# Kernel tuning notes

Hardware: AMD Instinct MI355X
Metric: run time of the kernel (lower is better)

## Reference

```python
import jax, jax.numpy as jnp
import numpy as np

B, C, H, W = 8, 256, 200, 200
N = 256
OUT = 7  # out_size


def setup_inputs() -> dict:
    key = jax.random.key(0)
    kf, kb = jax.random.split(key)
    feature_map = jax.random.normal(kf, (B, C, H, W), dtype=jnp.float32)
    # integer box coords; sort (lo,hi) pairs so x1<=x2, y1<=y2 as the torch
    # slicing semantics require for a non-empty ROI
    raw = jax.random.randint(kb, (B, N, 2, 2), 0, W)
    raw = jnp.sort(raw, axis=-1)
    x1 = raw[..., 0, 0]; x2 = raw[..., 0, 1]
    y1 = raw[..., 1, 0]; y2 = raw[..., 1, 1]
    proposals = jnp.stack([x1, y1, x2, y2], axis=-1).astype(jnp.int32)
    return {"feature_map": feature_map, "proposals": proposals}


def reference(feature_map, proposals):
    # Vectorized equivalent of: per-box clamp -> integer slice -> bilinear
    # F.interpolate(size=(OUT,OUT), align_corners=False).
    Bf, Cf, Hf, Wf = feature_map.shape
    S = OUT
    boxes = proposals.reshape(-1, 4)            # [R,4], R = B*N (loop order: batch, then box)
    R = boxes.shape[0]
    bx1 = jnp.clip(boxes[:, 0], 0, Wf - 1)
    by1 = jnp.clip(boxes[:, 1], 0, Hf - 1)
    bx2 = jnp.clip(boxes[:, 2], 0, Wf - 1)
    by2 = jnp.clip(boxes[:, 3], 0, Hf - 1)
    h = by2 - by1 + 1                            # ROI height (int)
    w = bx2 - bx1 + 1
    # PyTorch bilinear (align_corners=False): src = max((dst+0.5)*scale - 0.5, 0)
    grid = jnp.arange(S, dtype=jnp.float32) + 0.5           # [S]
    src_y = jnp.maximum(grid[None, :] * (h.astype(jnp.float32)[:, None] / S) - 0.5, 0.0)  # [R,S]
    src_x = jnp.maximum(grid[None, :] * (w.astype(jnp.float32)[:, None] / S) - 0.5, 0.0)
    y0f = jnp.floor(src_y); x0f = jnp.floor(src_x)
    wy = src_y - y0f; wx = src_x - x0f                       # bilinear lambdas [R,S]
    y0 = y0f.astype(jnp.int32); x0 = x0f.astype(jnp.int32)
    y1i = jnp.minimum(y0 + 1, (h - 1)[:, None])
    x1i = jnp.minimum(x0 + 1, (w - 1)[:, None])
    # absolute feature-map indices
    ya0 = by1[:, None] + y0;  ya1 = by1[:, None] + y1i       # [R,S]
    xa0 = bx1[:, None] + x0;  xa1 = bx1[:, None] + x1i
    bidx = jnp.arange(R, dtype=jnp.int32) // N               # [R] batch of each ROI
    fm = jnp.transpose(feature_map, (0, 2, 3, 1))            # [B,H,W,C] channels-last gather

    def gather(ya, xa):
        return fm[bidx[:, None, None], ya[:, :, None], xa[:, None, :]]  # [R,S,S,C]

    wy_ = wy[:, :, None, None]
    wx_ = wx[:, None, :, None]
    out = ((1 - wy_) * (1 - wx_) * gather(ya0, xa0)
           + (1 - wy_) * wx_ * gather(ya0, xa1)
           + wy_ * (1 - wx_) * gather(ya1, xa0)
           + wy_ * wx_ * gather(ya1, xa1))                    # [R,S,S,C]
    return jnp.transpose(out, (0, 3, 1, 2))                   # [R,C,S,S]
```

## Files before the change

### kernel.cpp

```cpp
#include <hip/hip_runtime.h>


#define C_DIM 256
#define H_DIM 200
#define W_DIM 200
#define S_DIM 7
#define N_ROI 256
#define NXCD  8

__global__ __launch_bounds__(256) void roialign_kernel(
    const float* __restrict__ fm,
    const int*   __restrict__ props,
    float*       __restrict__ out,
    int R)
{
    const int bid = blockIdx.x;
    const int r = (bid & (NXCD - 1)) * (R / NXCD) + (bid >> 3);
    const int b = r >> 8;

    int bx1 = props[r * 4 + 0];
    int by1 = props[r * 4 + 1];
    int bx2 = props[r * 4 + 2];
    int by2 = props[r * 4 + 3];
    bx1 = min(max(bx1, 0), W_DIM - 1);
    by1 = min(max(by1, 0), H_DIM - 1);
    bx2 = min(max(bx2, 0), W_DIM - 1);
    by2 = min(max(by2, 0), H_DIM - 1);
    const int h = by2 - by1 + 1;
    const int w = bx2 - bx1 + 1;

    const int l  = threadIdx.x & 63;
    const int wv = threadIdx.x >> 6;
    const bool active = (l < S_DIM * S_DIM);

    const int sy = l / 7;
    const int sx = l - sy * 7;

    float src_y = fmaxf(((float)sy + 0.5f) * (float)h * (1.0f / S_DIM) - 0.5f, 0.0f);
    float src_x = fmaxf(((float)sx + 0.5f) * (float)w * (1.0f / S_DIM) - 0.5f, 0.0f);
    const float y0f = floorf(src_y);
    const float x0f = floorf(src_x);
    const float wy = src_y - y0f;
    const float wx = src_x - x0f;
    const int y0 = (int)y0f;
    const int x0 = (int)x0f;
    const int y1 = min(y0 + 1, h - 1);
    const int x1 = min(x0 + 1, w - 1);
    const int ya0 = by1 + y0, ya1 = by1 + y1;
    const int xa0 = bx1 + x0, xa1 = bx1 + x1;

    const int o00 = ya0 * W_DIM + xa0;
    const int o01 = ya0 * W_DIM + xa1;
    const int o10 = ya1 * W_DIM + xa0;
    const int o11 = ya1 * W_DIM + xa1;
    const float w00 = (1.0f - wy) * (1.0f - wx);
    const float w01 = (1.0f - wy) * wx;
    const float w10 = wy * (1.0f - wx);
    const float w11 = wy * wx;

    const float* base = fm + ((size_t)b * C_DIM + wv) * (size_t)(H_DIM * W_DIM);
    float*       ob   = out + ((size_t)r * C_DIM + wv) * (S_DIM * S_DIM) + l;

    #pragma unroll 4
    for (int c = wv; c < C_DIM; c += 4) {
        if (active) {
            const float v00 = base[o00];
            const float v01 = base[o01];
            const float v10 = base[o10];
            const float v11 = base[o11];
            *ob = v00 * w00 + v01 * w01 + v10 * w10 + v11 * w11;
        }
        base += 4 * (size_t)(H_DIM * W_DIM);
        ob   += 4 * (S_DIM * S_DIM);
    }
}

extern "C" void kernel_launch(void* const* d_in, const int* in_sizes, int n_in,
                              void* d_out, int out_size, void* d_ws, size_t ws_size,
                              hipStream_t stream)
{
    const float* fm    = (const float*)d_in[0];
    const int*   props = (const int*)d_in[1];
    float*       out   = (float*)d_out;

    const int R = in_sizes[1] / 4;
    roialign_kernel<<<R, 256, 0, stream>>>(fm, props, out, R);
}
```

Measured before the change: 696.9 us.

## Stage half channel planes in LDS and compute all ROI bins per channel

The grid is reorganized so each block owns one (batch, channel, half-plane) tile instead of one ROI. The block streams 100 or 101 rows of the feature plane into LDS with float4 loads, then every thread loops over ROI×bin items and does the bilinear taps from LDS. Bins are split between the two halves by their top sample row. This replaces scattered global gathers, which re-read the same data many times, with one coalesced read of the feature map. In exchange, each block uses about 80 KB of LDS, which limits occupancy, output writes become strided across ROIs, and box and weight math is recomputed in every channel block.

```diff
diff --git a/kernel.cpp b/kernel.cpp
--- a/kernel.cpp
+++ b/kernel.cpp
@@ -1,77 +1,92 @@
 #include <hip/hip_runtime.h>
 
 
+#define B_DIM 8
 #define C_DIM 256
 #define H_DIM 200
 #define W_DIM 200
 #define S_DIM 7
-#define N_ROI 256
-#define NXCD  8
+#define NBINS (S_DIM * S_DIM)
+#define NROI  256
+#define THREADS 512
+#define ROWS_HALF0 101
+#define ROWS_HALF1 100
+#define LDS_BYTES (ROWS_HALF0 * W_DIM * 4)
 
-__global__ __launch_bounds__(256) void roialign_kernel(
+__global__ __launch_bounds__(THREADS) void roialign_kernel(
     const float* __restrict__ fm,
     const int*   __restrict__ props,
-    float*       __restrict__ out,
-    int R)
+    float*       __restrict__ out)
 {
-    const int bid = blockIdx.x;
-    const int r = (bid & (NXCD - 1)) * (R / NXCD) + (bid >> 3);
-    const int b = r >> 8;
+    extern __shared__ float sPlane[];
 
-    int bx1 = props[r * 4 + 0];
-    int by1 = props[r * 4 + 1];
-    int bx2 = props[r * 4 + 2];
-    int by2 = props[r * 4 + 3];
-    bx1 = min(max(bx1, 0), W_DIM - 1);
-    by1 = min(max(by1, 0), H_DIM - 1);
-    bx2 = min(max(bx2, 0), W_DIM - 1);
-    by2 = min(max(by2, 0), H_DIM - 1);
-    const int h = by2 - by1 + 1;
-    const int w = bx2 - bx1 + 1;
+    const int bid  = blockIdx.x;
+    const int half = bid & 1;
+    const int c    = (bid >> 1) & (C_DIM - 1);
+    const int b    = bid >> 9;
 
-    const int l  = threadIdx.x & 63;
-    const int wv = threadIdx.x >> 6;
-    const bool active = (l < S_DIM * S_DIM);
+    const int r0      = half ? 100 : 0;
+    const int nchunks = (half ? ROWS_HALF1 : ROWS_HALF0) * (W_DIM / 4);
 
-    const int sy = l / 7;
-    const int sx = l - sy * 7;
+    const int tid = threadIdx.x;
 
-    float src_y = fmaxf(((float)sy + 0.5f) * (float)h * (1.0f / S_DIM) - 0.5f, 0.0f);
-    float src_x = fmaxf(((float)sx + 0.5f) * (float)w * (1.0f / S_DIM) - 0.5f, 0.0f);
-    const float y0f = floorf(src_y);
-    const float x0f = floorf(src_x);
-    const float wy = src_y - y0f;
-    const float wx = src_x - x0f;
-    const int y0 = (int)y0f;
-    const int x0 = (int)x0f;
-    const int y1 = min(y0 + 1, h - 1);
-    const int x1 = min(x0 + 1, w - 1);
-    const int ya0 = by1 + y0, ya1 = by1 + y1;
-    const int xa0 = bx1 + x0, xa1 = bx1 + x1;
+    const float4* __restrict__ src =
+        (const float4*)(fm + ((size_t)(b * C_DIM + c)) * (H_DIM * W_DIM) + (size_t)r0 * W_DIM);
+    float4* dst = (float4*)sPlane;
+    for (int k = tid; k < nchunks; k += THREADS)
+        dst[k] = src[k];
+    __syncthreads();
 
-    const int o00 = ya0 * W_DIM + xa0;
-    const int o01 = ya0 * W_DIM + xa1;
-    const int o10 = ya1 * W_DIM + xa0;
-    const int o11 = ya1 * W_DIM + xa1;
-    const float w00 = (1.0f - wy) * (1.0f - wx);
-    const float w01 = (1.0f - wy) * wx;
-    const float w10 = wy * (1.0f - wx);
-    const float w11 = wy * wx;
+    const int4* __restrict__ pbase = (const int4*)props + (size_t)b * NROI;
 
-    const float* base = fm + ((size_t)b * C_DIM + wv) * (size_t)(H_DIM * W_DIM);
-    float*       ob   = out + ((size_t)r * C_DIM + wv) * (S_DIM * S_DIM) + l;
+    for (int item = tid; item < NROI * NBINS; item += THREADS) {
+        const int roi = item / NBINS;
+        const int bin = item - roi * NBINS;
+        const int sy  = bin / S_DIM;
+        const int sx  = bin - sy * S_DIM;
 
-    #pragma unroll 4
-    for (int c = wv; c < C_DIM; c += 4) {
-        if (active) {
-            const float v00 = base[o00];
-            const float v01 = base[o01];
-            const float v10 = base[o10];
-            const float v11 = base[o11];
-            *ob = v00 * w00 + v01 * w01 + v10 * w10 + v11 * w11;
-        }
-        base += 4 * (size_t)(H_DIM * W_DIM);
-        ob   += 4 * (S_DIM * S_DIM);
+        const int4 p = pbase[roi];
+        const int bx1 = min(max(p.x, 0), W_DIM - 1);
+        const int by1 = min(max(p.y, 0), H_DIM - 1);
+        const int bx2 = min(max(p.z, 0), W_DIM - 1);
+        const int by2 = min(max(p.w, 0), H_DIM - 1);
+        const int h = by2 - by1 + 1;
+        const int w = bx2 - bx1 + 1;
+
+        const float src_y = fmaxf(((float)sy + 0.5f) * (float)h * (1.0f / S_DIM) - 0.5f, 0.0f);
+        const float y0f = floorf(src_y);
+        const float wy  = src_y - y0f;
+        const int y0  = (int)y0f;
+        const int y1  = min(y0 + 1, h - 1);
+        const int ya0 = by1 + y0;
+        const int ya1 = by1 + y1;
+
+        const bool mine = half ? (ya0 >= 100) : (ya0 <= 99);
+        if (!mine) continue;
+
+        const float src_x = fmaxf(((float)sx + 0.5f) * (float)w * (1.0f / S_DIM) - 0.5f, 0.0f);
+        const float x0f = floorf(src_x);
+        const float wx  = src_x - x0f;
+        const int x0  = (int)x0f;
+        const int x1  = min(x0 + 1, w - 1);
+        const int xa0 = bx1 + x0;
+        const int xa1 = bx1 + x1;
+
+        const int ry0 = ya0 - r0;
+        const int ry1 = ya1 - r0;
+        const float v00 = sPlane[ry0 * W_DIM + xa0];
+        const float v01 = sPlane[ry0 * W_DIM + xa1];
+        const float v10 = sPlane[ry1 * W_DIM + xa0];
+        const float v11 = sPlane[ry1 * W_DIM + xa1];
+
+        const float w00 = (1.0f - wy) * (1.0f - wx);
+        const float w01 = (1.0f - wy) * wx;
+        const float w10 = wy * (1.0f - wx);
+        const float w11 = wy * wx;
+
+        const int r = b * NROI + roi;
+        out[((size_t)r * C_DIM + c) * NBINS + bin] =
+            v00 * w00 + v01 * w01 + v10 * w10 + v11 * w11;
     }
 }
 
@@ -83,6 +98,9 @@
     const int*   props = (const int*)d_in[1];
     float*       out   = (float*)d_out;
 
-    const int R = in_sizes[1] / 4;
-    roialign_kernel<<<R, 256, 0, stream>>>(fm, props, out, R);
+    hipFuncSetAttribute((const void*)roialign_kernel,
+                        hipFuncAttributeMaxDynamicSharedMemorySize, LDS_BYTES);
+
+    const int grid = B_DIM * C_DIM * 2;
+    roialign_kernel<<<grid, THREADS, LDS_BYTES, stream>>>(fm, props, out);
 }
```

Measured after the change: 557.5 us. -20.0%, faster.
